# Optimization experiments

Measured on AMD Instinct MI355X. Metric: run time of the kernel, lower is better.

Reference implementation:

```python
import jax, jax.numpy as jnp
import numpy as np

D = 1024; H = 16; K = 64; BK = 32; FFN = 4096; LORA = 48; CHUNK = 64
THETA_CLIP = float(np.pi / 2)
THETA_INIT = float(np.pi / 16)


def layernorm(x, g, b, eps=1e-6):
    m = x.mean(-1, keepdims=True)
    v = ((x - m) ** 2).mean(-1, keepdims=True)
    return (x - m) * jax.lax.rsqrt(v + eps) * g + b


def setup_inputs() -> dict:
    key = jax.random.key(0)
    ks = jax.random.split(key, 24)
    w = lambda k, s: jax.random.normal(k, s, jnp.float32) * 0.02
    return {
        "x": jax.random.normal(ks[0], (4, 2048, D), jnp.float32),
        "Wq": w(ks[1], (D, D)), "bq": jnp.zeros((D,), jnp.float32),
        "Wk": w(ks[2], (D, D)), "bk": jnp.zeros((D,), jnp.float32),
        "Wv": w(ks[3], (D, D)), "bv": jnp.zeros((D,), jnp.float32),
        "Wo": w(ks[4], (D, D)), "bo": jnp.zeros((D,), jnp.float32),
        "n1g": jnp.ones((D,), jnp.float32), "n1b": jnp.zeros((D,), jnp.float32),
        "n2g": jnp.ones((D,), jnp.float32), "n2b": jnp.zeros((D,), jnp.float32),
        "theta_base": jax.random.uniform(ks[5], (H, BK), jnp.float32, -THETA_INIT, THETA_INIT),
        "theta_w1": w(ks[6], (D, LORA)),
        "theta_w2": jax.random.uniform(ks[7], (LORA, H * BK), jnp.float32, -0.01, 0.01),
        "lambda_base": jax.random.uniform(ks[8], (H, BK), jnp.float32, 0.5, 6.0),
        "eta": jax.random.normal(ks[9], (H, BK), jnp.float32) * 0.1,
        "Wf1": w(ks[10], (D, FFN)), "bf1": jnp.zeros((FFN,), jnp.float32),
        "Wf2": w(ks[11], (FFN, D)), "bf2": jnp.zeros((D,), jnp.float32),
    }


def _forward(x, Wq, bq, Wk, bk, Wv, bv, Wo, bo, n1g, n1b, n2g, n2b,
             theta_base, theta_w1, theta_w2, lambda_base, eta, Wf1, bf1, Wf2, bf2):
    B, T, _ = x.shape
    NC = T // CHUNK
    xn = layernorm(x, n1g, n1b)
    # projections -> (B, H, T, K)
    q = (xn @ Wq + bq).reshape(B, T, H, K).transpose(0, 2, 1, 3)
    k = (xn @ Wk + bk).reshape(B, T, H, K).transpose(0, 2, 1, 3)
    v = (xn @ Wv + bv).reshape(B, T, H, K).transpose(0, 2, 1, 3)
    phi_k = jnp.where(k > 0, k + 1.0, jnp.exp(k))  # elu(k) + 1
    qp = q.reshape(B, H, T, BK, 2)
    kp = phi_k.reshape(B, H, T, BK, 2)
    q_c = jax.lax.complex(qp[..., 0], qp[..., 1])  # (B,H,T,BK) complex64
    k_c = jax.lax.complex(kp[..., 0], kp[..., 1])
    # data-dependent rotation angles via LoRA
    lora = jnp.tanh(xn @ theta_w1) @ theta_w2  # (B,T,H*BK)
    theta = theta_base[None, None] + lora.reshape(B, T, H, BK)
    theta = jnp.clip(theta, -THETA_CLIP, THETA_CLIP).transpose(0, 2, 1, 3)  # (B,H,T,BK)
    lam = lambda_base[None, :, None, :] + eta[None, :, None, :] * theta ** 2
    log_z = jax.lax.complex(-lam, theta)  # complex log-decay per step

    def chunks(a):  # (B,H,T,...) -> (NC,B,H,CHUNK,...)
        return jnp.moveaxis(a.reshape(B, H, NC, CHUNK, *a.shape[3:]), 2, 0)

    tril = jnp.tril(jnp.ones((CHUNK, CHUNK), bool))[None, None, :, :, None]

    def step(c, inputs):
        lz, kc, qc, vf = inputs  # (B,H,tc,BK)x3, (B,H,tc,K)
        cumlog = jnp.cumsum(lz, axis=2)
        diff = cumlog[:, :, :, None, :] - cumlog[:, :, None, :, :]  # (B,H,tc,tc,BK)
        real = jnp.where(tril, diff.real, -60.0)
        A = jnp.where(tril, jnp.exp(jax.lax.complex(real, diff.imag)),
                      jnp.zeros((), jnp.complex64))
        scaled_k = A * kc[:, :, None, :, :]
        S_intra = jnp.einsum('bhtsk,bhsv->bhtkv', scaled_k, vf.astype(jnp.complex64))
        decay = jnp.exp(cumlog)
        S_total = decay[..., None] * c[:, :, None] + S_intra  # (B,H,tc,BK,K)
        y = jnp.einsum('bhtk,bhtkv->bhtv', jnp.conj(qc), S_total).real
        return S_total[:, :, -1], y

    c0 = jnp.zeros((B, H, BK, K), jnp.complex64)
    _, ys = jax.lax.scan(step, c0, (chunks(log_z), chunks(k_c), chunks(q_c), chunks(v)))
    out = jnp.moveaxis(ys, 0, 2).reshape(B, H, T, K)
    attn = out.transpose(0, 2, 1, 3).reshape(B, T, D) @ Wo + bo
    x1 = x + attn
    h = layernorm(x1, n2g, n2b)
    return x1 + jax.nn.gelu(h @ Wf1 + bf1) @ Wf2 + bf2


def reference(x, Wq, bq, Wk, bk, Wv, bv, Wo, bo, n1g, n1b, n2g, n2b,
              theta_base, theta_w1, theta_w2, lambda_base, eta, Wf1, bf1, Wf2, bf2):
    return _forward(x, Wq, bq, Wk, bk, Wv, bv, Wo, bo, n1g, n1b, n2g, n2b,
                    theta_base, theta_w1, theta_w2, lambda_base, eta, Wf1, bf1, Wf2, bf2)
```

## Files before the change

### kernel.cpp

```cpp
#include <hip/hip_runtime.h>


#define QS 3328

typedef __bf16 bf16x8 __attribute__((ext_vector_type(8)));
typedef float f32x4 __attribute__((ext_vector_type(4)));

__device__ __forceinline__ unsigned short f2bf(float f) {
  unsigned int u = __builtin_bit_cast(unsigned int, f);
  u += 0x7FFFu + ((u >> 16) & 1u);
  return (unsigned short)(u >> 16);
}
__device__ __forceinline__ float bf2f(unsigned short u) {
  unsigned int x = ((unsigned int)u) << 16;
  return __builtin_bit_cast(float, x);
}
__device__ __forceinline__ unsigned int pack2(float a, float b) {
  return (unsigned int)f2bf(a) | ((unsigned int)f2bf(b) << 16);
}

__device__ __forceinline__ void gload_lds16(const void* g, void* l) {
  __builtin_amdgcn_global_load_lds((const __attribute__((address_space(1))) void*)g,
                                   (__attribute__((address_space(3))) void*)l, 16, 0, 0);
}

__device__ __forceinline__ float gelu_tanh(float v) {
  const float z = 0.7978845608028654f * fmaf(0.044715f * v * v, v, v);
  const float e = __expf(2.f * z);
  return 0.5f * v * (2.f - 2.f / (1.f + e));
}

__global__ void fill_kernel(float* p, float v, int n) {
  int i = blockIdx.x * 256 + threadIdx.x;
  if (i < n) p[i] = v;
}

__global__ __launch_bounds__(256) void ln_kernel(
    const float* __restrict__ x, const float* __restrict__ g,
    const float* __restrict__ b, unsigned short* __restrict__ out) {
  const int row = blockIdx.x, tid = threadIdx.x;
  float4 v = ((const float4*)(x + (size_t)row * 1024))[tid];
  float s = v.x + v.y + v.z + v.w;
  float sq = v.x * v.x + v.y * v.y + v.z * v.z + v.w * v.w;
#pragma unroll
  for (int o = 32; o > 0; o >>= 1) { s += __shfl_xor(s, o); sq += __shfl_xor(sq, o); }
  __shared__ float red[8];
  const int wid = tid >> 6;
  if ((tid & 63) == 0) { red[wid] = s; red[4 + wid] = sq; }
  __syncthreads();
  s = red[0] + red[1] + red[2] + red[3];
  sq = red[4] + red[5] + red[6] + red[7];
  const float mean = s * (1.f / 1024.f);
  const float var = sq * (1.f / 1024.f) - mean * mean;
  const float rstd = rsqrtf(var + 1e-6f);
  float4 gv = ((const float4*)g)[tid];
  float4 bvv = ((const float4*)b)[tid];
  ushort4 o4;
  o4.x = f2bf((v.x - mean) * rstd * gv.x + bvv.x);
  o4.y = f2bf((v.y - mean) * rstd * gv.y + bvv.y);
  o4.z = f2bf((v.z - mean) * rstd * gv.z + bvv.z);
  o4.w = f2bf((v.w - mean) * rstd * gv.w + bvv.w);
  *(ushort4*)(out + (size_t)row * 1024 + tid * 4) = o4;
}

__global__ __launch_bounds__(256) void transpose_bf16(
    const float* __restrict__ src, unsigned short* __restrict__ dst, int K, int N) {
  __shared__ float tile[32][33];
  const int n0 = blockIdx.x * 32, k0 = blockIdx.y * 32;
  const int tx = threadIdx.x, ty = threadIdx.y;
#pragma unroll
  for (int j = 0; j < 32; j += 8) tile[tx][ty + j] = src[(size_t)(k0 + ty + j) * N + n0 + tx];
  __syncthreads();
#pragma unroll
  for (int j = 0; j < 32; j += 8)
    dst[(size_t)(n0 + ty + j) * K + k0 + tx] = f2bf(tile[ty + j][tx]);
}

__global__ __launch_bounds__(256) void prep_wcat(
    const float* __restrict__ Wq, const float* __restrict__ Wk,
    const float* __restrict__ Wv, const float* __restrict__ tw1,
    unsigned short* __restrict__ dst) {
  __shared__ float tile[32][33];
  const int r0 = blockIdx.x * 32, c0 = blockIdx.y * 32;
  const int tx = threadIdx.x, ty = threadIdx.y;
  const int r = r0 + tx;
#pragma unroll
  for (int j = 0; j < 32; j += 8) {
    const int c = c0 + ty + j;
    float v;
    if (r < 1024) v = Wq[(size_t)c * 1024 + r];
    else if (r < 2048) v = Wk[(size_t)c * 1024 + (r - 1024)];
    else if (r < 3072) v = Wv[(size_t)c * 1024 + (r - 2048)];
    else if (r < 3120) v = tw1[(size_t)c * 48 + (r - 3072)];
    else v = 0.f;
    tile[tx][ty + j] = v;
  }
  __syncthreads();
#pragma unroll
  for (int j = 0; j < 32; j += 8)
    dst[(size_t)(r0 + ty + j) * 1024 + c0 + tx] = f2bf(tile[ty + j][tx]);
}

__global__ void biascat_kernel(const float* bq, const float* bk, const float* bv, float* dst) {
  int i = blockIdx.x * 256 + threadIdx.x;
  if (i >= QS) return;
  float v = 0.f;
  if (i < 1024) v = bq[i];
  else if (i < 2048) v = bk[i - 1024];
  else if (i < 3072) v = bv[i - 2048];
  dst[i] = v;
}

template <int MODE>
__global__ __launch_bounds__(512, 2) void gemm8p_kernel(
    const unsigned short* __restrict__ A, const unsigned short* __restrict__ BT,
    const float* __restrict__ bias, void* __restrict__ out,
    int N, int Kstride, int Klen) {
  __shared__ __align__(16) unsigned short SA[2][2][8192];
  __shared__ __align__(16) unsigned short SB[2][2][8192];
  const int nwg = gridDim.x * gridDim.y;
  int d = blockIdx.y * gridDim.x + blockIdx.x;
  d = (d & 7) * (nwg >> 3) + (d >> 3);
  const int n0 = (d % gridDim.x) * 256, m0 = (d / gridDim.x) * 256;

  const int tid = threadIdx.x, wv = tid >> 6, ln = tid & 63;
  const int wm = wv >> 2, wn = wv & 3;
  const int l15 = ln & 15, hi4 = ln >> 4;

  const unsigned short* Abase = A + (size_t)m0 * Kstride;
  const unsigned short* Bbase = BT + (size_t)n0 * Kstride;

  const int srow = ln >> 3;
  const int skg = (ln & 7) ^ srow;
  const unsigned short* ga00 = Abase + (size_t)((0 * 8 + wv) * 8 + srow) * Kstride + skg * 8;
  const unsigned short* ga01 = Abase + (size_t)((1 * 8 + wv) * 8 + srow) * Kstride + skg * 8;
  const unsigned short* ga10 = Abase + (size_t)(128 + (0 * 8 + wv) * 8 + srow) * Kstride + skg * 8;
  const unsigned short* ga11 = Abase + (size_t)(128 + (1 * 8 + wv) * 8 + srow) * Kstride + skg * 8;
  const unsigned short* gb00 = Bbase + (size_t)((0 * 8 + wv) * 8 + srow) * Kstride + skg * 8;
  const unsigned short* gb01 = Bbase + (size_t)((1 * 8 + wv) * 8 + srow) * Kstride + skg * 8;
  const unsigned short* gb10 = Bbase + (size_t)(128 + (0 * 8 + wv) * 8 + srow) * Kstride + skg * 8;
  const unsigned short* gb11 = Bbase + (size_t)(128 + (1 * 8 + wv) * 8 + srow) * Kstride + skg * 8;

  auto STA = [&](int pbuf) {
    gload_lds16(ga00, (char*)SA + pbuf * 32768 + wv * 1024);
    gload_lds16(ga01, (char*)SA + pbuf * 32768 + (8 + wv) * 1024);
    gload_lds16(ga10, (char*)SA + pbuf * 32768 + 16384 + wv * 1024);
    gload_lds16(ga11, (char*)SA + pbuf * 32768 + 16384 + (8 + wv) * 1024);
    ga00 += 64; ga01 += 64; ga10 += 64; ga11 += 64;
  };
  auto STB = [&](int pbuf) {
    gload_lds16(gb00, (char*)SB + pbuf * 32768 + wv * 1024);
    gload_lds16(gb01, (char*)SB + pbuf * 32768 + (8 + wv) * 1024);
    gload_lds16(gb10, (char*)SB + pbuf * 32768 + 16384 + wv * 1024);
    gload_lds16(gb11, (char*)SB + pbuf * 32768 + 16384 + (8 + wv) * 1024);
    gb00 += 64; gb01 += 64; gb10 += 64; gb11 += 64;
  };

  const int x7 = l15 & 7;
  const char* aA0 = (const char*)SA + wm * 16384 + l15 * 128 + ((hi4 ^ x7) * 16);
  const char* aA1 = (const char*)SA + wm * 16384 + l15 * 128 + (((4 + hi4) ^ x7) * 16);
  const char* aB0 = (const char*)SB + (wn >> 1) * 16384 + (wn & 1) * 8192 + l15 * 128 + ((hi4 ^ x7) * 16);
  const char* aB1 = (const char*)SB + (wn >> 1) * 16384 + (wn & 1) * 8192 + l15 * 128 + (((4 + hi4) ^ x7) * 16);

  f32x4 acc[8][4] = {};
  const int nt = Klen >> 6;

  STA(0);
  STB(0);
  STA(1);
  asm volatile("s_waitcnt vmcnt(4)" ::: "memory");
  __builtin_amdgcn_s_barrier();

#define GTILE(P, T)                                                            \
  {                                                                            \
    if ((T) + 1 < nt) STB((P) ^ 1);                                            \
    bf16x8 bfr0[4], bfr1[4];                                                   \
    _Pragma("unroll")                                                          \
    for (int fn = 0; fn < 4; ++fn) {                                           \
      bfr0[fn] = *(const bf16x8*)(aB0 + (P) * 32768 + fn * 2048);              \
      bfr1[fn] = *(const bf16x8*)(aB1 + (P) * 32768 + fn * 2048);              \
    }                                                                          \
    _Pragma("unroll")                                                          \
    for (int q = 0; q < 8; ++q) {                                              \
      bf16x8 a0 = *(const bf16x8*)(aA0 + (P) * 32768 + q * 2048);              \
      bf16x8 a1 = *(const bf16x8*)(aA1 + (P) * 32768 + q * 2048);              \
      __builtin_amdgcn_s_setprio(1);                                           \
      _Pragma("unroll")                                                        \
      for (int fn = 0; fn < 4; ++fn) {                                         \
        acc[q][fn] = __builtin_amdgcn_mfma_f32_16x16x32_bf16(a0, bfr0[fn],     \
                                                             acc[q][fn], 0, 0, 0); \
        acc[q][fn] = __builtin_amdgcn_mfma_f32_16x16x32_bf16(a1, bfr1[fn],     \
                                                             acc[q][fn], 0, 0, 0); \
      }                                                                        \
      __builtin_amdgcn_s_setprio(0);                                           \
    }                                                                          \
    __builtin_amdgcn_s_barrier();                                              \
    if ((T) + 2 < nt) STA(P);                                                  \
    if ((T) + 1 < nt) {                                                        \
      if ((T) + 2 < nt) asm volatile("s_waitcnt vmcnt(4)" ::: "memory");       \
      else              asm volatile("s_waitcnt vmcnt(0)" ::: "memory");       \
      __builtin_amdgcn_s_barrier();                                            \
    }                                                                          \
  }

  for (int t = 0; t < nt; t += 2) {
    GTILE(0, t);
    GTILE(1, t + 1);
  }
#undef GTILE

#pragma unroll
  for (int fm = 0; fm < 8; ++fm) {
#pragma unroll
    for (int fn = 0; fn < 4; ++fn) {
      const int row = m0 + wm * 128 + fm * 16 + hi4 * 4;
      const int col = n0 + wn * 64 + fn * 16 + l15;
      const float bval = bias[col];
#pragma unroll
      for (int r = 0; r < 4; ++r) {
        const float v = acc[fm][fn][r] + bval;
        const size_t oi = (size_t)(row + r) * N + col;
        if constexpr (MODE == 2) {
          ((unsigned short*)out)[oi] = f2bf(gelu_tanh(v));
        } else {
          ((unsigned short*)out)[oi] = f2bf(v);
        }
      }
    }
  }
}

__global__ __launch_bounds__(512, 2) void gemm8pn_kernel(
    const unsigned short* __restrict__ A, const unsigned short* __restrict__ BT,
    const float* __restrict__ bias, const float* __restrict__ res,
    float* __restrict__ out, int N, int Kstride, int Klen) {
  __shared__ __align__(16) unsigned short SA[2][2][8192];
  __shared__ __align__(16) unsigned short SB[2][8192];
  const int nwg = gridDim.x * gridDim.y;
  int d = blockIdx.y * gridDim.x + blockIdx.x;
  d = (d & 7) * (nwg >> 3) + (d >> 3);
  const int n0 = (d % gridDim.x) * 128, m0 = (d / gridDim.x) * 256;

  const int tid = threadIdx.x, wv = tid >> 6, ln = tid & 63;
  const int wm = wv >> 1, wn = wv & 1;
  const int l15 = ln & 15, hi4 = ln >> 4;

  const unsigned short* Abase = A + (size_t)m0 * Kstride;
  const unsigned short* Bbase = BT + (size_t)n0 * Kstride;

  const int srow = ln >> 3;
  const int skg = (ln & 7) ^ srow;
  const unsigned short* ga00 = Abase + (size_t)((0 * 8 + wv) * 8 + srow) * Kstride + skg * 8;
  const unsigned short* ga01 = Abase + (size_t)((1 * 8 + wv) * 8 + srow) * Kstride + skg * 8;
  const unsigned short* ga10 = Abase + (size_t)(128 + (0 * 8 + wv) * 8 + srow) * Kstride + skg * 8;
  const unsigned short* ga11 = Abase + (size_t)(128 + (1 * 8 + wv) * 8 + srow) * Kstride + skg * 8;
  const unsigned short* gb0 = Bbase + (size_t)((0 * 8 + wv) * 8 + srow) * Kstride + skg * 8;
  const unsigned short* gb1 = Bbase + (size_t)((1 * 8 + wv) * 8 + srow) * Kstride + skg * 8;

  auto STA = [&](int pbuf) {
    gload_lds16(ga00, (char*)SA + pbuf * 32768 + wv * 1024);
    gload_lds16(ga01, (char*)SA + pbuf * 32768 + (8 + wv) * 1024);
    gload_lds16(ga10, (char*)SA + pbuf * 32768 + 16384 + wv * 1024);
    gload_lds16(ga11, (char*)SA + pbuf * 32768 + 16384 + (8 + wv) * 1024);
    ga00 += 64; ga01 += 64; ga10 += 64; ga11 += 64;
  };
  auto STB = [&](int pbuf) {
    gload_lds16(gb0, (char*)SB + pbuf * 16384 + wv * 1024);
    gload_lds16(gb1, (char*)SB + pbuf * 16384 + (8 + wv) * 1024);
    gb0 += 64; gb1 += 64;
  };

  const int x7 = l15 & 7;
  const char* aA0 = (const char*)SA + (wm >> 1) * 16384 + (wm & 1) * 8192 + l15 * 128 + ((hi4 ^ x7) * 16);
  const char* aA1 = (const char*)SA + (wm >> 1) * 16384 + (wm & 1) * 8192 + l15 * 128 + (((4 + hi4) ^ x7) * 16);
  const char* aB0 = (const char*)SB + wn * 8192 + l15 * 128 + ((hi4 ^ x7) * 16);
  const char* aB1 = (const char*)SB + wn * 8192 + l15 * 128 + (((4 + hi4) ^ x7) * 16);

  f32x4 acc[4][4] = {};
  const int nt = Klen >> 6;

  STA(0);
  STB(0);
  STA(1);
  asm volatile("s_waitcnt vmcnt(4)" ::: "memory");
  __builtin_amdgcn_s_barrier();

#define GTILEN(P, T)                                                           \
  {                                                                            \
    if ((T) + 1 < nt) STB((P) ^ 1);                                            \
    bf16x8 bfr0[4], bfr1[4];                                                   \
    _Pragma("unroll")                                                          \
    for (int fn = 0; fn < 4; ++fn) {                                           \
      bfr0[fn] = *(const bf16x8*)(aB0 + (P) * 16384 + fn * 2048);              \
      bfr1[fn] = *(const bf16x8*)(aB1 + (P) * 16384 + fn * 2048);              \
    }                                                                          \
    _Pragma("unroll")                                                          \
    for (int q = 0; q < 4; ++q) {                                              \
      bf16x8 a0 = *(const bf16x8*)(aA0 + (P) * 32768 + q * 2048);              \
      bf16x8 a1 = *(const bf16x8*)(aA1 + (P) * 32768 + q * 2048);              \
      __builtin_amdgcn_s_setprio(1);                                           \
      _Pragma("unroll")                                                        \
      for (int fn = 0; fn < 4; ++fn) {                                         \
        acc[q][fn] = __builtin_amdgcn_mfma_f32_16x16x32_bf16(a0, bfr0[fn],     \
                                                             acc[q][fn], 0, 0, 0); \
        acc[q][fn] = __builtin_amdgcn_mfma_f32_16x16x32_bf16(a1, bfr1[fn],     \
                                                             acc[q][fn], 0, 0, 0); \
      }                                                                        \
      __builtin_amdgcn_s_setprio(0);                                           \
    }                                                                          \
    __builtin_amdgcn_s_barrier();                                              \
    if ((T) + 2 < nt) STA(P);                                                  \
    if ((T) + 1 < nt) {                                                        \
      if ((T) + 2 < nt) asm volatile("s_waitcnt vmcnt(4)" ::: "memory");       \
      else              asm volatile("s_waitcnt vmcnt(0)" ::: "memory");       \
      __builtin_amdgcn_s_barrier();                                            \
    }                                                                          \
  }

  for (int t = 0; t < nt; t += 2) {
    GTILEN(0, t);
    GTILEN(1, t + 1);
  }
#undef GTILEN

#pragma unroll
  for (int fm = 0; fm < 4; ++fm) {
#pragma unroll
    for (int fn = 0; fn < 4; ++fn) {
      const int row = m0 + wm * 64 + fm * 16 + hi4 * 4;
      const int col = n0 + wn * 64 + fn * 16 + l15;
      const float bval = bias[col];
#pragma unroll
      for (int r = 0; r < 4; ++r) {
        const size_t oi = (size_t)(row + r) * N + col;
        out[oi] = acc[fm][fn][r] + bval + res[oi];
      }
    }
  }
}

__global__ __launch_bounds__(256) void lora2_kernel(
    const unsigned short* __restrict__ qkv, const float* __restrict__ w2,
    const float* __restrict__ tbase, float* __restrict__ theta) {
  __shared__ float lt[8][48];
  const int m0 = blockIdx.x * 32;
  const int tid = threadIdx.x;
  const int col = tid * 2;
  const float tb0 = tbase[col], tb1 = tbase[col + 1];
  for (int grp = 0; grp < 4; ++grp) {
    const int mg = m0 + grp * 8;
    __syncthreads();
    for (int idx = tid; idx < 384; idx += 256) {
      const int tok = idx / 48, jj = idx % 48;
      lt[tok][jj] = tanhf(bf2f(qkv[(size_t)(mg + tok) * QS + 3072 + jj]));
    }
    __syncthreads();
    float a0[8], a1[8];
#pragma unroll
    for (int tok = 0; tok < 8; ++tok) { a0[tok] = tb0; a1[tok] = tb1; }
    for (int jj = 0; jj < 48; ++jj) {
      const float2 w = *(const float2*)&w2[(size_t)jj * 512 + col];
#pragma unroll
      for (int tok = 0; tok < 8; ++tok) {
        const float l = lt[tok][jj];
        a0[tok] = fmaf(l, w.x, a0[tok]);
        a1[tok] = fmaf(l, w.y, a1[tok]);
      }
    }
    const float CL = 1.5707963267948966f;
#pragma unroll
    for (int tok = 0; tok < 8; ++tok) {
      float c0 = fminf(fmaxf(a0[tok], -CL), CL);
      float c1 = fminf(fmaxf(a1[tok], -CL), CL);
      *(float2*)&theta[(size_t)(mg + tok) * 512 + col] = make_float2(c0, c1);
    }
  }
}

__global__ __launch_bounds__(256) void attn_intra(
    const unsigned short* __restrict__ qkv, const float* __restrict__ theta,
    const float* __restrict__ lamb, const float* __restrict__ eta,
    float* __restrict__ yi, unsigned short* __restrict__ QG,
    unsigned short* __restrict__ TCG, float* __restrict__ Dg) {
  const int c = blockIdx.x, bh = blockIdx.y;
  const int b = bh >> 4, h = bh & 15;
  const int tid = threadIdx.x, wv = tid >> 6, lane = tid & 63;
  const int sc = c * 4 + wv;
  const int cid = bh * 128 + sc;
  const int mw = b * 2048 + sc * 16;

  __shared__ unsigned short QDm[4][16][64];
  __shared__ unsigned short KDm[4][16][64];
  __shared__ unsigned short KdET[4][64][32];
  __shared__ unsigned short VT[4][64][32];
  __shared__ unsigned short Gs[4][16][32];

  {
    unsigned int* kz = (unsigned int*)&KdET[wv][0][0];
    unsigned int* vz = (unsigned int*)&VT[wv][0][0];
    for (int idx = lane; idx < 512; idx += 64) {
      const int r = idx >> 3, p = (idx & 7) + 8;
      kz[r * 16 + p] = 0; vz[r * 16 + p] = 0;
    }
    unsigned int* gz = (unsigned int*)&Gs[wv][0][0];
    for (int idx = lane; idx < 128; idx += 64) {
      const int r = idx >> 3, p = (idx & 7) + 8;
      gz[r * 16 + p] = 0;
    }
  }
  for (int ss = 0; ss < 16; ++ss)
    VT[wv][lane][ss] = qkv[(size_t)(mw + ss) * QS + 2048 + h * 64 + lane];

  const int bk = lane & 31, th = lane >> 5;
  const float lb = lamb[h * 32 + bk], et = eta[h * 32 + bk];
  float L[8], Th[8], qr[8], qi[8], kr[8], ki[8];
  float runL = 0.f, runT = 0.f;
#pragma unroll
  for (int i = 0; i < 8; ++i) {
    const size_t m = (size_t)(mw + th * 8 + i);
    const float tv = theta[m * 512 + h * 32 + bk];
    const float lam = fmaf(et * tv, tv, lb);
    runL += lam; L[i] = runL;
    runT += tv;  Th[i] = runT;
    const unsigned int qp = *(const unsigned int*)&qkv[m * QS + h * 64 + 2 * bk];
    const unsigned int kp = *(const unsigned int*)&qkv[m * QS + 1024 + h * 64 + 2 * bk];
    qr[i] = bf2f((unsigned short)(qp & 0xFFFF)); qi[i] = bf2f((unsigned short)(qp >> 16));
    const float kx = bf2f((unsigned short)(kp & 0xFFFF));
    const float ky = bf2f((unsigned short)(kp >> 16));
    kr[i] = kx > 0.f ? kx + 1.f : __expf(kx);
    ki[i] = ky > 0.f ? ky + 1.f : __expf(ky);
  }
  const float oL = __shfl_xor(runL, 32), oT = __shfl_xor(runT, 32);
  const float Lm = th ? oL : runL;
  const float Tm = th ? oT : runT;
  const float Ltot = runL + oL, Ttot = runT + oT;
  const float Lbase = th ? oL : 0.f, Tbase = th ? oT : 0.f;
  float Es, Ec; __sincosf(Tm, &Es, &Ec);
  const float Ee = __expf(-Lm);
  const float Er = Ee * Ec, Ei = Ee * Es;
  float Fs, Fc; __sincosf(Ttot - Tm, &Fs, &Fc);
  const float Fe = __expf(-(Ltot - Lm));
  const float Fr = Fe * Fc, Fi = Fe * Fs;
  if (th == 0) {
    float Ds, Dc; __sincosf(Ttot, &Ds, &Dc);
    const float De = __expf(-Ltot);
    *(float2*)&Dg[((size_t)cid * 32 + bk) * 2] = make_float2(De * Dc, De * Ds);
  }
  unsigned int* qd32 = (unsigned int*)&QDm[wv][0][0];
  unsigned int* kd32 = (unsigned int*)&KDm[wv][0][0];
#pragma unroll
  for (int i = 0; i < 8; ++i) {
    const int t = th * 8 + i;
    const float Lg = Lbase + L[i], Tg = Tbase + Th[i];
    const float dm = __expf(-(Lg - Lm));
    float sn, cs; __sincosf(Tg - Tm, &sn, &cs);
    const float qmr = dm * (qr[i] * cs + qi[i] * sn);
    const float qmi = dm * (qr[i] * sn - qi[i] * cs);
    const float rd = 1.f / dm;
    const float kmr = rd * (kr[i] * cs + ki[i] * sn);
    const float kmi = rd * (ki[i] * cs - kr[i] * sn);
    const int sidx = (t * 32 + bk) ^ ((t & 7) << 2);
    qd32[sidx] = pack2(qmr, qmi);
    kd32[sidx] = pack2(kmr, -kmi);
    ((unsigned int*)QG)[(size_t)cid * 512 + t * 32 + bk] =
        pack2(qmr * Er - qmi * Ei, qmr * Ei + qmi * Er);
    const float er = kmr * Fr - kmi * Fi;
    const float ei = kmr * Fi + kmi * Fr;
    KdET[wv][bk][t] = f2bf(er);
    KdET[wv][32 + bk][t] = f2bf(ei);
  }

  const int l15 = lane & 15, hi = lane >> 4;
  const char* qb = (const char*)&QDm[wv][0][0];
  const char* kb = (const char*)&KDm[wv][0][0];
  f32x4 z = {};
  f32x4 g = z;
  {
    bf16x8 a0 = *(const bf16x8*)(qb + l15 * 128 + ((16 * hi) ^ ((l15 & 7) << 4)));
    bf16x8 b0 = *(const bf16x8*)(kb + l15 * 128 + ((16 * hi) ^ ((l15 & 7) << 4)));
    bf16x8 a1 = *(const bf16x8*)(qb + l15 * 128 + ((64 + 16 * hi) ^ ((l15 & 7) << 4)));
    bf16x8 b1 = *(const bf16x8*)(kb + l15 * 128 + ((64 + 16 * hi) ^ ((l15 & 7) << 4)));
    g = __builtin_amdgcn_mfma_f32_16x16x32_bf16(a0, b0, g, 0, 0, 0);
    g = __builtin_amdgcn_mfma_f32_16x16x32_bf16(a1, b1, g, 0, 0, 0);
  }
#pragma unroll
  for (int r = 0; r < 4; ++r) {
    const float gv = (l15 <= 4 * hi + r) ? g[r] : 0.f;
    Gs[wv][4 * hi + r][l15] = f2bf(gv);
  }
  const char* gsb = (const char*)&Gs[wv][0][0];
  const char* vtb = (const char*)&VT[wv][0][0];
  bf16x8 aG = *(const bf16x8*)(gsb + l15 * 64 + 16 * hi);
#pragma unroll
  for (int nt = 0; nt < 4; ++nt) {
    bf16x8 bV = *(const bf16x8*)(vtb + (nt * 16 + l15) * 64 + 16 * hi);
    f32x4 y = __builtin_amdgcn_mfma_f32_16x16x32_bf16(aG, bV, z, 0, 0, 0);
#pragma unroll
    for (int r = 0; r < 4; ++r)
      yi[(size_t)cid * 1024 + (4 * hi + r) * 64 + nt * 16 + l15] = y[r];
  }
  const char* keb = (const char*)&KdET[wv][0][0];
#pragma unroll
  for (int mt = 0; mt < 4; ++mt) {
    bf16x8 aT = *(const bf16x8*)(keb + (mt * 16 + l15) * 64 + 16 * hi);
#pragma unroll
    for (int nt = 0; nt < 4; ++nt) {
      bf16x8 bV = *(const bf16x8*)(vtb + (nt * 16 + l15) * 64 + 16 * hi);
      f32x4 t4 = __builtin_amdgcn_mfma_f32_16x16x32_bf16(aT, bV, z, 0, 0, 0);
#pragma unroll
      for (int r = 0; r < 4; ++r)
        TCG[(size_t)cid * 4096 + (mt * 16 + 4 * hi + r) * 64 + nt * 16 + l15] = f2bf(t4[r]);
    }
  }
}

__global__ __launch_bounds__(256) void scanB_kernel(
    const unsigned short* __restrict__ TCG, const float* __restrict__ Dg,
    unsigned int* __restrict__ CPACK) {
  const int bh = blockIdx.x & 63, g = blockIdx.x >> 6;
  const int tid = threadIdx.x;
  const int v = tid & 63, bk = g * 4 + (tid >> 6);
  const size_t base = (size_t)bh * 128;
  float Cr = 0.f, Ci = 0.f;
  float trx[4], tix[4]; float2 dx[4];
  auto LOADQ = [&](int c0, float* tr, float* ti, float2* dd) {
#pragma unroll
    for (int u = 0; u < 4; ++u) {
      const size_t cid = base + c0 + u;
      tr[u] = bf2f(TCG[cid * 4096 + bk * 64 + v]);
      ti[u] = bf2f(TCG[cid * 4096 + (32 + bk) * 64 + v]);
      dd[u] = *(const float2*)&Dg[(cid * 32 + bk) * 2];
    }
  };
  LOADQ(0, trx, tix, dx);
  for (int c0 = 0; c0 < 128; c0 += 4) {
    float tra[4], tia[4]; float2 da[4];
#pragma unroll
    for (int u = 0; u < 4; ++u) { tra[u] = trx[u]; tia[u] = tix[u]; da[u] = dx[u]; }
    if (c0 + 4 < 128) LOADQ(c0 + 4, trx, tix, dx);
#pragma unroll
    for (int u = 0; u < 4; ++u) {
      CPACK[(base + c0 + u) * 2048 + bk * 64 + v] = pack2(Cr, -Ci);
      const float nr = fmaf(da[u].x, Cr, fmaf(-da[u].y, Ci, tra[u]));
      const float ni = fmaf(da[u].x, Ci, fmaf(da[u].y, Cr, tia[u]));
      Cr = nr; Ci = ni;
    }
  }
}

__global__ __launch_bounds__(256) void attn_cross(
    const float* __restrict__ yi, const unsigned short* __restrict__ QG,
    const unsigned int* __restrict__ CPACK, unsigned short* __restrict__ attn) {
  const int c = blockIdx.x, bh = blockIdx.y;
  const int b = bh >> 4, h = bh & 15;
  const int tid = threadIdx.x, wv = tid >> 6, lane = tid & 63;
  const int sc = c * 4 + wv, cid = bh * 128 + sc;
  const int mw = b * 2048 + sc * 16;
  __shared__ unsigned short Cp[4][64][64];
  __shared__ unsigned short Qs[4][16][64];
  unsigned int* cp32 = (unsigned int*)&Cp[wv][0][0];
  const unsigned int* cg = CPACK + (size_t)cid * 2048;
  for (int bkq = 0; bkq < 32; ++bkq) {
    cp32[(lane * 32 + bkq) ^ ((lane & 7) << 2)] = cg[bkq * 64 + lane];
  }
  unsigned int* qs32 = (unsigned int*)&Qs[wv][0][0];
  const unsigned int* qg = (const unsigned int*)QG + (size_t)cid * 512;
  for (int ii = 0; ii < 8; ++ii) {
    const int flat = ii * 64 + lane;
    const int row = flat >> 5, col = flat & 31;
    qs32[(row * 32 + col) ^ ((row & 7) << 2)] = qg[flat];
  }
  const int l15 = lane & 15, hi = lane >> 4;
  const char* qb = (const char*)&Qs[wv][0][0];
  const char* cb = (const char*)&Cp[wv][0][0];
  bf16x8 a0 = *(const bf16x8*)(qb + l15 * 128 + ((16 * hi) ^ ((l15 & 7) << 4)));
  bf16x8 a1 = *(const bf16x8*)(qb + l15 * 128 + ((64 + 16 * hi) ^ ((l15 & 7) << 4)));
  f32x4 z = {};
#pragma unroll
  for (int nt = 0; nt < 4; ++nt) {
    const int vr = nt * 16 + l15;
    bf16x8 b0 = *(const bf16x8*)(cb + vr * 128 + ((16 * hi) ^ ((vr & 7) << 4)));
    bf16x8 b1 = *(const bf16x8*)(cb + vr * 128 + ((64 + 16 * hi) ^ ((vr & 7) << 4)));
    f32x4 y = __builtin_amdgcn_mfma_f32_16x16x32_bf16(a0, b0, z, 0, 0, 0);
    y = __builtin_amdgcn_mfma_f32_16x16x32_bf16(a1, b1, y, 0, 0, 0);
#pragma unroll
    for (int r = 0; r < 4; ++r) {
      const int t = 4 * hi + r;
      const float out = y[r] + yi[(size_t)cid * 1024 + t * 64 + vr];
      attn[(size_t)(mw + t) * 1024 + h * 64 + vr] = f2bf(out);
    }
  }
}

extern "C" void kernel_launch(void* const* d_in, const int* in_sizes, int n_in,
                              void* d_out, int out_size, void* d_ws, size_t ws_size,
                              hipStream_t stream) {
  const float* x   = (const float*)d_in[0];
  const float* Wq  = (const float*)d_in[1];
  const float* bq  = (const float*)d_in[2];
  const float* Wk  = (const float*)d_in[3];
  const float* bk_ = (const float*)d_in[4];
  const float* Wv  = (const float*)d_in[5];
  const float* bv  = (const float*)d_in[6];
  const float* Wo  = (const float*)d_in[7];
  const float* bo  = (const float*)d_in[8];
  const float* n1g = (const float*)d_in[9];
  const float* n1b = (const float*)d_in[10];
  const float* n2g = (const float*)d_in[11];
  const float* n2b = (const float*)d_in[12];
  const float* thb = (const float*)d_in[13];
  const float* tw1 = (const float*)d_in[14];
  const float* tw2 = (const float*)d_in[15];
  const float* lamb= (const float*)d_in[16];
  const float* eta = (const float*)d_in[17];
  const float* Wf1 = (const float*)d_in[18];
  const float* bf1 = (const float*)d_in[19];
  const float* Wf2 = (const float*)d_in[20];
  const float* bf2 = (const float*)d_in[21];

  char* ws = (char*)d_ws;
  size_t off = 0;
  auto alloc = [&](size_t bytes) {
    size_t r = off;
    off += (bytes + 255) & ~(size_t)255;
    return r;
  };
  unsigned short* WCAT = (unsigned short*)(ws + alloc((size_t)QS * 1024 * 2));
  unsigned short* WOT  = (unsigned short*)(ws + alloc(1024ull * 1024 * 2));
  unsigned short* WF1T = (unsigned short*)(ws + alloc(4096ull * 1024 * 2));
  unsigned short* WF2T = (unsigned short*)(ws + alloc(1024ull * 4096 * 2));
  float* BIASC = (float*)(ws + alloc((size_t)QS * 4));
  unsigned short* XN = (unsigned short*)(ws + alloc(8192ull * 1024 * 2));
  char* QKVbase = ws + alloc(8192ull * 4096 * 2);
  unsigned short* QKV = (unsigned short*)QKVbase;
  unsigned int* CPACK = (unsigned int*)QKVbase;
  unsigned short* GBUF = (unsigned short*)QKVbase;
  float* THETA = (float*)(ws + alloc(8192ull * 512 * 4));
  unsigned short* ATTN = (unsigned short*)THETA;
  float* YI = (float*)(ws + alloc(8192ull * 1024 * 4));
  float* X1 = YI;
  unsigned short* QG = (unsigned short*)(ws + alloc(8192ull * 1024 * 2));
  unsigned short* TCG = (unsigned short*)(ws + alloc(8192ull * 4096 * 2));
  float* DG = (float*)(ws + alloc(8192ull * 32 * 2 * 4));

  if (ws_size < off) {
    fill_kernel<<<dim3((out_size + 255) / 256), dim3(256), 0, stream>>>((float*)d_out, 12345.0f, out_size);
    return;
  }

  const dim3 b256(256), b32x8(32, 8), b512(512);

  prep_wcat<<<dim3(104, 32), b32x8, 0, stream>>>(Wq, Wk, Wv, tw1, WCAT);
  transpose_bf16<<<dim3(32, 32), b32x8, 0, stream>>>(Wo, WOT, 1024, 1024);
  transpose_bf16<<<dim3(128, 32), b32x8, 0, stream>>>(Wf1, WF1T, 1024, 4096);
  transpose_bf16<<<dim3(32, 128), b32x8, 0, stream>>>(Wf2, WF2T, 4096, 1024);
  biascat_kernel<<<dim3(13), b256, 0, stream>>>(bq, bk_, bv, BIASC);

  ln_kernel<<<dim3(8192), b256, 0, stream>>>(x, n1g, n1b, XN);
  gemm8p_kernel<3><<<dim3(13, 32), b512, 0, stream>>>(XN, WCAT, BIASC, QKV, QS, 1024, 1024);
  lora2_kernel<<<dim3(256), b256, 0, stream>>>(QKV, tw2, thb, THETA);
  attn_intra<<<dim3(32, 64), b256, 0, stream>>>(QKV, THETA, lamb, eta, YI, QG, TCG, DG);
  scanB_kernel<<<dim3(512), b256, 0, stream>>>(TCG, DG, CPACK);
  attn_cross<<<dim3(32, 64), b256, 0, stream>>>(YI, QG, CPACK, ATTN);
  gemm8pn_kernel<<<dim3(8, 32), b512, 0, stream>>>(ATTN, WOT, bo, x, X1, 1024, 1024, 1024);
  ln_kernel<<<dim3(8192), b256, 0, stream>>>(X1, n2g, n2b, XN);
  gemm8p_kernel<2><<<dim3(16, 32), b512, 0, stream>>>(XN, WF1T, bf1, GBUF, 4096, 1024, 1024);
  gemm8pn_kernel<<<dim3(8, 32), b512, 0, stream>>>(GBUF, WF2T, bf2, X1, (float*)d_out, 1024, 4096, 4096);
}
```

Measured before the change: 436.3 us.

## Use 32x32x16 MFMA in GEMMs and merge weight-prep kernels into one launch

Both GEMM kernels switch from 16x16x32 bf16 MFMA tiles to 32x32x16 tiles with 16-element accumulators, so fewer LDS fragment reads are issued per MFMA and operands are reused more. The epilogue row mapping is rewritten to match the 32x32 output layout. Separately, the weight-transpose, concat and bias-concat prep kernels are fused into a single launch to cut launch overhead. The new mapping risks layout mistakes and LDS bank conflicts under the existing swizzle.

```diff
diff --git a/kernel.cpp b/kernel.cpp
--- a/kernel.cpp
+++ b/kernel.cpp
@@ -5,6 +5,7 @@
 
 typedef __bf16 bf16x8 __attribute__((ext_vector_type(8)));
 typedef float f32x4 __attribute__((ext_vector_type(4)));
+typedef float f32x16 __attribute__((ext_vector_type(16)));
 
 __device__ __forceinline__ unsigned short f2bf(float f) {
   unsigned int u = __builtin_bit_cast(unsigned int, f);
@@ -63,11 +64,11 @@
   *(ushort4*)(out + (size_t)row * 1024 + tid * 4) = o4;
 }
 
-__global__ __launch_bounds__(256) void transpose_bf16(
-    const float* __restrict__ src, unsigned short* __restrict__ dst, int K, int N) {
+__device__ __forceinline__ void tr_tile(
+    const float* __restrict__ src, unsigned short* __restrict__ dst,
+    int K, int N, int bx, int by, int tx, int ty) {
   __shared__ float tile[32][33];
-  const int n0 = blockIdx.x * 32, k0 = blockIdx.y * 32;
-  const int tx = threadIdx.x, ty = threadIdx.y;
+  const int n0 = bx * 32, k0 = by * 32;
 #pragma unroll
   for (int j = 0; j < 32; j += 8) tile[tx][ty + j] = src[(size_t)(k0 + ty + j) * N + n0 + tx];
   __syncthreads();
@@ -76,39 +77,57 @@
     dst[(size_t)(n0 + ty + j) * K + k0 + tx] = f2bf(tile[ty + j][tx]);
 }
 
-__global__ __launch_bounds__(256) void prep_wcat(
+__global__ __launch_bounds__(256) void prep_all(
     const float* __restrict__ Wq, const float* __restrict__ Wk,
     const float* __restrict__ Wv, const float* __restrict__ tw1,
-    unsigned short* __restrict__ dst) {
-  __shared__ float tile[32][33];
-  const int r0 = blockIdx.x * 32, c0 = blockIdx.y * 32;
-  const int tx = threadIdx.x, ty = threadIdx.y;
-  const int r = r0 + tx;
-#pragma unroll
-  for (int j = 0; j < 32; j += 8) {
-    const int c = c0 + ty + j;
-    float v;
-    if (r < 1024) v = Wq[(size_t)c * 1024 + r];
-    else if (r < 2048) v = Wk[(size_t)c * 1024 + (r - 1024)];
-    else if (r < 3072) v = Wv[(size_t)c * 1024 + (r - 2048)];
-    else if (r < 3120) v = tw1[(size_t)c * 48 + (r - 3072)];
-    else v = 0.f;
-    tile[tx][ty + j] = v;
-  }
-  __syncthreads();
-#pragma unroll
-  for (int j = 0; j < 32; j += 8)
-    dst[(size_t)(r0 + ty + j) * 1024 + c0 + tx] = f2bf(tile[ty + j][tx]);
-}
-
-__global__ void biascat_kernel(const float* bq, const float* bk, const float* bv, float* dst) {
-  int i = blockIdx.x * 256 + threadIdx.x;
-  if (i >= QS) return;
-  float v = 0.f;
-  if (i < 1024) v = bq[i];
-  else if (i < 2048) v = bk[i - 1024];
-  else if (i < 3072) v = bv[i - 2048];
-  dst[i] = v;
+    const float* __restrict__ Wo, const float* __restrict__ Wf1,
+    const float* __restrict__ Wf2,
+    const float* __restrict__ bq, const float* __restrict__ bk,
+    const float* __restrict__ bv,
+    unsigned short* __restrict__ WCAT, unsigned short* __restrict__ WOT,
+    unsigned short* __restrict__ WF1T, unsigned short* __restrict__ WF2T,
+    float* __restrict__ BIASC) {
+  const int id = blockIdx.x;
+  const int tx = threadIdx.x & 31, ty = threadIdx.x >> 5;
+  if (id < 3328) {
+    __shared__ float tile[32][33];
+    const int bx = id % 104, by = id / 104;
+    const int r0 = bx * 32, c0 = by * 32;
+    const int r = r0 + tx;
+#pragma unroll
+    for (int j = 0; j < 32; j += 8) {
+      const int c = c0 + ty + j;
+      float v;
+      if (r < 1024) v = Wq[(size_t)c * 1024 + r];
+      else if (r < 2048) v = Wk[(size_t)c * 1024 + (r - 1024)];
+      else if (r < 3072) v = Wv[(size_t)c * 1024 + (r - 2048)];
+      else if (r < 3120) v = tw1[(size_t)c * 48 + (r - 3072)];
+      else v = 0.f;
+      tile[tx][ty + j] = v;
+    }
+    __syncthreads();
+#pragma unroll
+    for (int j = 0; j < 32; j += 8)
+      WCAT[(size_t)(r0 + ty + j) * 1024 + c0 + tx] = f2bf(tile[ty + j][tx]);
+  } else if (id < 4352) {
+    const int i2 = id - 3328;
+    tr_tile(Wo, WOT, 1024, 1024, i2 % 32, i2 / 32, tx, ty);
+  } else if (id < 8448) {
+    const int i3 = id - 4352;
+    tr_tile(Wf1, WF1T, 1024, 4096, i3 % 128, i3 / 128, tx, ty);
+  } else if (id < 12544) {
+    const int i4 = id - 8448;
+    tr_tile(Wf2, WF2T, 4096, 1024, i4 % 32, i4 / 32, tx, ty);
+  } else {
+    const int i5 = (id - 12544) * 256 + threadIdx.x;
+    if (i5 < QS) {
+      float v = 0.f;
+      if (i5 < 1024) v = bq[i5];
+      else if (i5 < 2048) v = bk[i5 - 1024];
+      else if (i5 < 3072) v = bv[i5 - 2048];
+      BIASC[i5] = v;
+    }
+  }
 }
 
 template <int MODE>
@@ -125,7 +144,7 @@
 
   const int tid = threadIdx.x, wv = tid >> 6, ln = tid & 63;
   const int wm = wv >> 2, wn = wv & 3;
-  const int l15 = ln & 15, hi4 = ln >> 4;
+  const int l31 = ln & 31, hi5 = ln >> 5;
 
   const unsigned short* Abase = A + (size_t)m0 * Kstride;
   const unsigned short* Bbase = BT + (size_t)n0 * Kstride;
@@ -156,13 +175,17 @@
     gb00 += 64; gb01 += 64; gb10 += 64; gb11 += 64;
   };
 
-  const int x7 = l15 & 7;
-  const char* aA0 = (const char*)SA + wm * 16384 + l15 * 128 + ((hi4 ^ x7) * 16);
-  const char* aA1 = (const char*)SA + wm * 16384 + l15 * 128 + (((4 + hi4) ^ x7) * 16);
-  const char* aB0 = (const char*)SB + (wn >> 1) * 16384 + (wn & 1) * 8192 + l15 * 128 + ((hi4 ^ x7) * 16);
-  const char* aB1 = (const char*)SB + (wn >> 1) * 16384 + (wn & 1) * 8192 + l15 * 128 + (((4 + hi4) ^ x7) * 16);
-
-  f32x4 acc[8][4] = {};
+  const int x7 = l31 & 7;
+  const char* aAk[4];
+  const char* aBk[4];
+#pragma unroll
+  for (int ks = 0; ks < 4; ++ks) {
+    const int ko = ((ks * 2 + hi5) ^ x7) * 16;
+    aAk[ks] = (const char*)SA + wm * 16384 + l31 * 128 + ko;
+    aBk[ks] = (const char*)SB + (wn >> 1) * 16384 + (wn & 1) * 8192 + l31 * 128 + ko;
+  }
+
+  f32x16 acc[4][2] = {};
   const int nt = Klen >> 6;
 
   STA(0);
@@ -174,24 +197,23 @@
 #define GTILE(P, T)                                                            \
   {                                                                            \
     if ((T) + 1 < nt) STB((P) ^ 1);                                            \
-    bf16x8 bfr0[4], bfr1[4];                                                   \
     _Pragma("unroll")                                                          \
-    for (int fn = 0; fn < 4; ++fn) {                                           \
-      bfr0[fn] = *(const bf16x8*)(aB0 + (P) * 32768 + fn * 2048);              \
-      bfr1[fn] = *(const bf16x8*)(aB1 + (P) * 32768 + fn * 2048);              \
-    }                                                                          \
-    _Pragma("unroll")                                                          \
-    for (int q = 0; q < 8; ++q) {                                              \
-      bf16x8 a0 = *(const bf16x8*)(aA0 + (P) * 32768 + q * 2048);              \
-      bf16x8 a1 = *(const bf16x8*)(aA1 + (P) * 32768 + q * 2048);              \
+    for (int ks = 0; ks < 4; ++ks) {                                           \
+      bf16x8 b0 = *(const bf16x8*)(aBk[ks] + (P) * 32768);                     \
+      bf16x8 b1 = *(const bf16x8*)(aBk[ks] + (P) * 32768 + 4096);              \
+      bf16x8 a0 = *(const bf16x8*)(aAk[ks] + (P) * 32768);                     \
+      bf16x8 a1 = *(const bf16x8*)(aAk[ks] + (P) * 32768 + 4096);              \
+      bf16x8 a2 = *(const bf16x8*)(aAk[ks] + (P) * 32768 + 8192);              \
+      bf16x8 a3 = *(const bf16x8*)(aAk[ks] + (P) * 32768 + 12288);             \
       __builtin_amdgcn_s_setprio(1);                                           \
-      _Pragma("unroll")                                                        \
-      for (int fn = 0; fn < 4; ++fn) {                                         \
-        acc[q][fn] = __builtin_amdgcn_mfma_f32_16x16x32_bf16(a0, bfr0[fn],     \
-                                                             acc[q][fn], 0, 0, 0); \
-        acc[q][fn] = __builtin_amdgcn_mfma_f32_16x16x32_bf16(a1, bfr1[fn],     \
-                                                             acc[q][fn], 0, 0, 0); \
-      }                                                                        \
+      acc[0][0] = __builtin_amdgcn_mfma_f32_32x32x16_bf16(a0, b0, acc[0][0], 0, 0, 0); \
+      acc[0][1] = __builtin_amdgcn_mfma_f32_32x32x16_bf16(a0, b1, acc[0][1], 0, 0, 0); \
+      acc[1][0] = __builtin_amdgcn_mfma_f32_32x32x16_bf16(a1, b0, acc[1][0], 0, 0, 0); \
+      acc[1][1] = __builtin_amdgcn_mfma_f32_32x32x16_bf16(a1, b1, acc[1][1], 0, 0, 0); \
+      acc[2][0] = __builtin_amdgcn_mfma_f32_32x32x16_bf16(a2, b0, acc[2][0], 0, 0, 0); \
+      acc[2][1] = __builtin_amdgcn_mfma_f32_32x32x16_bf16(a2, b1, acc[2][1], 0, 0, 0); \
+      acc[3][0] = __builtin_amdgcn_mfma_f32_32x32x16_bf16(a3, b0, acc[3][0], 0, 0, 0); \
+      acc[3][1] = __builtin_amdgcn_mfma_f32_32x32x16_bf16(a3, b1, acc[3][1], 0, 0, 0); \
       __builtin_amdgcn_s_setprio(0);                                           \
     }                                                                          \
     __builtin_amdgcn_s_barrier();                                              \
@@ -210,16 +232,16 @@
 #undef GTILE
 
 #pragma unroll
-  for (int fm = 0; fm < 8; ++fm) {
-#pragma unroll
-    for (int fn = 0; fn < 4; ++fn) {
-      const int row = m0 + wm * 128 + fm * 16 + hi4 * 4;
-      const int col = n0 + wn * 64 + fn * 16 + l15;
+  for (int mr = 0; mr < 4; ++mr) {
+#pragma unroll
+    for (int nr = 0; nr < 2; ++nr) {
+      const int col = n0 + wn * 64 + nr * 32 + l31;
       const float bval = bias[col];
 #pragma unroll
-      for (int r = 0; r < 4; ++r) {
-        const float v = acc[fm][fn][r] + bval;
-        const size_t oi = (size_t)(row + r) * N + col;
+      for (int reg = 0; reg < 16; ++reg) {
+        const int row = m0 + wm * 128 + mr * 32 + (reg & 3) + 8 * (reg >> 2) + 4 * hi5;
+        const float v = acc[mr][nr][reg] + bval;
+        const size_t oi = (size_t)row * N + col;
         if constexpr (MODE == 2) {
           ((unsigned short*)out)[oi] = f2bf(gelu_tanh(v));
         } else {
@@ -243,7 +265,7 @@
 
   const int tid = threadIdx.x, wv = tid >> 6, ln = tid & 63;
   const int wm = wv >> 1, wn = wv & 1;
-  const int l15 = ln & 15, hi4 = ln >> 4;
+  const int l31 = ln & 31, hi5 = ln >> 5;
 
   const unsigned short* Abase = A + (size_t)m0 * Kstride;
   const unsigned short* Bbase = BT + (size_t)n0 * Kstride;
@@ -270,13 +292,17 @@
     gb0 += 64; gb1 += 64;
   };
 
-  const int x7 = l15 & 7;
-  const char* aA0 = (const char*)SA + (wm >> 1) * 16384 + (wm & 1) * 8192 + l15 * 128 + ((hi4 ^ x7) * 16);
-  const char* aA1 = (const char*)SA + (wm >> 1) * 16384 + (wm & 1) * 8192 + l15 * 128 + (((4 + hi4) ^ x7) * 16);
-  const char* aB0 = (const char*)SB + wn * 8192 + l15 * 128 + ((hi4 ^ x7) * 16);
-  const char* aB1 = (const char*)SB + wn * 8192 + l15 * 128 + (((4 + hi4) ^ x7) * 16);
-
-  f32x4 acc[4][4] = {};
+  const int x7 = l31 & 7;
+  const char* aAk[4];
+  const char* aBk[4];
+#pragma unroll
+  for (int ks = 0; ks < 4; ++ks) {
+    const int ko = ((ks * 2 + hi5) ^ x7) * 16;
+    aAk[ks] = (const char*)SA + (wm >> 1) * 16384 + (wm & 1) * 8192 + l31 * 128 + ko;
+    aBk[ks] = (const char*)SB + wn * 8192 + l31 * 128 + ko;
+  }
+
+  f32x16 acc[2][2] = {};
   const int nt = Klen >> 6;
 
   STA(0);
@@ -288,24 +314,17 @@
 #define GTILEN(P, T)                                                           \
   {                                                                            \
     if ((T) + 1 < nt) STB((P) ^ 1);                                            \
-    bf16x8 bfr0[4], bfr1[4];                                                   \
     _Pragma("unroll")                                                          \
-    for (int fn = 0; fn < 4; ++fn) {                                           \
-      bfr0[fn] = *(const bf16x8*)(aB0 + (P) * 16384 + fn * 2048);              \
-      bfr1[fn] = *(const bf16x8*)(aB1 + (P) * 16384 + fn * 2048);              \
-    }                                                                          \
-    _Pragma("unroll")                                                          \
-    for (int q = 0; q < 4; ++q) {                                              \
-      bf16x8 a0 = *(const bf16x8*)(aA0 + (P) * 32768 + q * 2048);              \
-      bf16x8 a1 = *(const bf16x8*)(aA1 + (P) * 32768 + q * 2048);              \
+    for (int ks = 0; ks < 4; ++ks) {                                           \
+      bf16x8 b0 = *(const bf16x8*)(aBk[ks] + (P) * 16384);                     \
+      bf16x8 b1 = *(const bf16x8*)(aBk[ks] + (P) * 16384 + 4096);              \
+      bf16x8 a0 = *(const bf16x8*)(aAk[ks] + (P) * 32768);                     \
+      bf16x8 a1 = *(const bf16x8*)(aAk[ks] + (P) * 32768 + 4096);              \
       __builtin_amdgcn_s_setprio(1);                                           \
-      _Pragma("unroll")                                                        \
-      for (int fn = 0; fn < 4; ++fn) {                                         \
-        acc[q][fn] = __builtin_amdgcn_mfma_f32_16x16x32_bf16(a0, bfr0[fn],     \
-                                                             acc[q][fn], 0, 0, 0); \
-        acc[q][fn] = __builtin_amdgcn_mfma_f32_16x16x32_bf16(a1, bfr1[fn],     \
-                                                             acc[q][fn], 0, 0, 0); \
-      }                                                                        \
+      acc[0][0] = __builtin_amdgcn_mfma_f32_32x32x16_bf16(a0, b0, acc[0][0], 0, 0, 0); \
+      acc[0][1] = __builtin_amdgcn_mfma_f32_32x32x16_bf16(a0, b1, acc[0][1], 0, 0, 0); \
+      acc[1][0] = __builtin_amdgcn_mfma_f32_32x32x16_bf16(a1, b0, acc[1][0], 0, 0, 0); \
+      acc[1][1] = __builtin_amdgcn_mfma_f32_32x32x16_bf16(a1, b1, acc[1][1], 0, 0, 0); \
       __builtin_amdgcn_s_setprio(0);                                           \
     }                                                                          \
     __builtin_amdgcn_s_barrier();                                              \
@@ -324,16 +343,16 @@
 #undef GTILEN
 
 #pragma unroll
-  for (int fm = 0; fm < 4; ++fm) {
-#pragma unroll
-    for (int fn = 0; fn < 4; ++fn) {
-      const int row = m0 + wm * 64 + fm * 16 + hi4 * 4;
-      const int col = n0 + wn * 64 + fn * 16 + l15;
+  for (int mr = 0; mr < 2; ++mr) {
+#pragma unroll
+    for (int nr = 0; nr < 2; ++nr) {
+      const int col = n0 + wn * 64 + nr * 32 + l31;
       const float bval = bias[col];
 #pragma unroll
-      for (int r = 0; r < 4; ++r) {
-        const size_t oi = (size_t)(row + r) * N + col;
-        out[oi] = acc[fm][fn][r] + bval + res[oi];
+      for (int reg = 0; reg < 16; ++reg) {
+        const int row = m0 + wm * 64 + mr * 32 + (reg & 3) + 8 * (reg >> 2) + 4 * hi5;
+        const size_t oi = (size_t)row * N + col;
+        out[oi] = acc[mr][nr][reg] + bval + res[oi];
       }
     }
   }
@@ -648,13 +667,10 @@
     return;
   }
 
-  const dim3 b256(256), b32x8(32, 8), b512(512);
-
-  prep_wcat<<<dim3(104, 32), b32x8, 0, stream>>>(Wq, Wk, Wv, tw1, WCAT);
-  transpose_bf16<<<dim3(32, 32), b32x8, 0, stream>>>(Wo, WOT, 1024, 1024);
-  transpose_bf16<<<dim3(128, 32), b32x8, 0, stream>>>(Wf1, WF1T, 1024, 4096);
-  transpose_bf16<<<dim3(32, 128), b32x8, 0, stream>>>(Wf2, WF2T, 4096, 1024);
-  biascat_kernel<<<dim3(13), b256, 0, stream>>>(bq, bk_, bv, BIASC);
+  const dim3 b256(256), b512(512);
+
+  prep_all<<<dim3(12557), b256, 0, stream>>>(Wq, Wk, Wv, tw1, Wo, Wf1, Wf2,
+                                             bq, bk_, bv, WCAT, WOT, WF1T, WF2T, BIASC);
 
   ln_kernel<<<dim3(8192), b256, 0, stream>>>(x, n1g, n1b, XN);
   gemm8p_kernel<3><<<dim3(13, 32), b512, 0, stream>>>(XN, WCAT, BIASC, QKV, QS, 1024, 1024);
```

Result: no change. 430.0 us, median of 2 (-1.4%).
